# Performance work log

Measured on AMD Instinct MI355X. Metric: run time of the kernel, lower is better.

Reference implementation:

```python
import jax, jax.numpy as jnp
import numpy as np

NHEADS = 16


def setup_inputs() -> dict:
    key = jax.random.key(0)
    ks = jax.random.split(key, 5)
    B, S, D = 2, 2048, 1024
    x = jax.random.normal(ks[0], (B, S, D), dtype=jnp.float32)
    W_packed = jax.random.normal(ks[1], (3 * D, D), dtype=jnp.float32) * (1.0 / np.sqrt(D))
    b_packed = jax.random.normal(ks[2], (3 * D,), dtype=jnp.float32) * 0.02
    W_out = jax.random.normal(ks[3], (D, D), dtype=jnp.float32) * (1.0 / np.sqrt(D))
    b_out = jax.random.normal(ks[4], (D,), dtype=jnp.float32) * 0.02
    return {"x": x, "W_packed": W_packed, "b_packed": b_packed, "W_out": W_out, "b_out": b_out}


def reference(x, W_packed, b_packed, W_out, b_out):
    B, S, D = x.shape
    H = NHEADS
    hd = D // H
    # packed QKV projection (self-attention: q is k is v)
    qkv = x @ W_packed.T + b_packed                       # [B,S,3D]
    q, k, v = jnp.split(qkv, 3, axis=-1)

    def heads(t):
        return t.reshape(B, S, H, hd).transpose(0, 2, 1, 3)  # [B,H,S,hd]

    q, k, v = map(heads, (q, k, v))

    # ALiBi slopes per flex path: exp2(-(h+1)*8/H)
    slopes = jnp.exp2(-(jnp.arange(1, H + 1, dtype=x.dtype) * (8.0 / H)))  # [H]
    pos = jnp.arange(S)
    rel = (pos[None, :] - pos[:, None]).astype(x.dtype)    # kv_idx - q_idx, [S,S]
    bias = slopes[:, None, None] * rel                     # [H,S,S]
    causal = pos[None, :] <= pos[:, None]                  # allowed positions
    neg = jnp.finfo(x.dtype).min
    attn_mask = jnp.where(causal[None, :, :], bias, neg)   # [H,S,S]

    scale = 1.0 / np.sqrt(hd)
    scores = jnp.einsum("bhqd,bhkd->bhqk", q, k) * scale + attn_mask[None]
    attn = jax.nn.softmax(scores, axis=-1)
    out = jnp.einsum("bhqk,bhkd->bhqd", attn, v)           # [B,H,S,hd]
    out = out.transpose(0, 2, 1, 3).reshape(B, S, D)
    return out @ W_out.T + b_out
```

## Files before the change

### kernel.cpp

```cpp
#include <hip/hip_runtime.h>

typedef float f32x4 __attribute__((ext_vector_type(4)));
typedef __bf16 bf16x8 __attribute__((ext_vector_type(8)));
typedef unsigned short u16;

__device__ __forceinline__ f32x4 mfma16(bf16x8 a, bf16x8 b, f32x4 c) {
  return __builtin_amdgcn_mfma_f32_16x16x32_bf16(a, b, c, 0, 0, 0);
}

__device__ __forceinline__ void gll16(const void* g, void* l) {
  __builtin_amdgcn_global_load_lds(
      (const __attribute__((address_space(1))) void*)g,
      (__attribute__((address_space(3))) void*)l, 16, 0, 0);
}

__global__ void cvt3_kernel(const float* __restrict__ x,
                            const float* __restrict__ wp,
                            const float* __restrict__ wo,
                            __bf16* __restrict__ out) {
  int idx = blockIdx.x * blockDim.x + threadIdx.x;
  int stride = gridDim.x * blockDim.x;
  for (int i = idx; i < 1048576; i += stride) {
    const float* src;
    if (i < 524288) src = x + (size_t)i * 8;
    else if (i < 917504) src = wp + (size_t)(i - 524288) * 8;
    else src = wo + (size_t)(i - 917504) * 8;
    f32x4 a = *(const f32x4*)src;
    f32x4 b = *(const f32x4*)(src + 4);
    bf16x8 r;
#pragma unroll
    for (int j = 0; j < 4; ++j) {
      r[j] = (__bf16)a[j];
      r[4 + j] = (__bf16)b[j];
    }
    *(bf16x8*)(out + (size_t)i * 8) = r;
  }
}

template <int BM, int BN, int MODE>
__global__ __launch_bounds__(256, 3) void gemm_bt(
    const u16* __restrict__ A, const u16* __restrict__ B,
    const float* __restrict__ bias, float* __restrict__ Cout,
    __bf16* __restrict__ qb, __bf16* __restrict__ kp, __bf16* __restrict__ vp,
    int M, int N, int K, int mtiles) {
  constexpr int MREP = BM / 32;
  constexpr int NREP = BN / 32;
  constexpr int LA = BM / 64;
  constexpr int LB = BN / 64;
  static_assert(LA + LB == 4, "vmcnt literals assume 4 loads/wave/step");
  __shared__ u16 lA[3 * BM * 32];
  __shared__ u16 lB[3 * BN * 32];
  const int tid = threadIdx.x;
  const int wid = tid >> 6;
  const int lane = tid & 63;
  const int lr = lane & 15;
  const int lg = lane >> 4;

  const int nwg = gridDim.x;
  const int lid = blockIdx.x;
  const int sw = (lid & 7) * (nwg >> 3) + (lid >> 3);
  const int bm = (sw % mtiles) * BM;
  const int bn = (sw / mtiles) * BN;
  const int wm = (wid >> 1) * (BM / 2);
  const int wn = (wid & 1) * (BN / 2);

  f32x4 acc[MREP][NREP] = {};

  auto stage = [&](int bf, int t) {
    const int kt = t * 32;
    char* baseA = (char*)lA + bf * (BM * 64);
    char* baseB = (char*)lB + bf * (BN * 64);
#pragma unroll
    for (int j = 0; j < LA; ++j) {
      int i16 = tid + j * 256;
      int row = i16 >> 2;
      int c = ((i16 & 3) - (row >> 1)) & 3;
      gll16(A + (size_t)(bm + row) * K + kt + c * 8, baseA + i16 * 16);
    }
#pragma unroll
    for (int j = 0; j < LB; ++j) {
      int i16 = tid + j * 256;
      int row = i16 >> 2;
      int c = ((i16 & 3) - (row >> 1)) & 3;
      gll16(B + (size_t)(bn + row) * K + kt + c * 8, baseB + i16 * 16);
    }
  };

  const int T = K / 32;
  stage(0, 0);
  stage(1, 1);
  stage(2, 2);

  const int slotA = ((lg + (lr >> 1)) & 3) * 8;

  for (int t = 0; t < T; ++t) {
    const int rem = T - 1 - t;
    if (rem >= 2)
      asm volatile("s_waitcnt vmcnt(8)" ::: "memory");
    else if (rem == 1)
      asm volatile("s_waitcnt vmcnt(4)" ::: "memory");
    else
      asm volatile("s_waitcnt vmcnt(0)" ::: "memory");
    __builtin_amdgcn_s_barrier();

    const u16* cA = lA + (t % 3) * BM * 32;
    const u16* cB = lB + (t % 3) * BN * 32;
    bf16x8 af[MREP], bfr[NREP];
#pragma unroll
    for (int mt = 0; mt < MREP; ++mt)
      af[mt] = *(const bf16x8*)&cA[(wm + mt * 16 + lr) * 32 + slotA];
#pragma unroll
    for (int nt = 0; nt < NREP; ++nt)
      bfr[nt] = *(const bf16x8*)&cB[(wn + nt * 16 + lr) * 32 + slotA];
#pragma unroll
    for (int mt = 0; mt < MREP; ++mt)
#pragma unroll
      for (int nt = 0; nt < NREP; ++nt)
        acc[mt][nt] = mfma16(af[mt], bfr[nt], acc[mt][nt]);

    __builtin_amdgcn_sched_barrier(0);
    __builtin_amdgcn_s_barrier();
    if (t + 3 < T) stage(t % 3, t + 3);
  }

#pragma unroll
  for (int nt = 0; nt < NREP; ++nt) {
    int col = bn + wn + nt * 16 + lr;
    float bv = bias[col];
#pragma unroll
    for (int mt = 0; mt < MREP; ++mt) {
#pragma unroll
      for (int r = 0; r < 4; ++r) {
        int row = bm + wm + mt * 16 + lg * 4 + r;
        float val = acc[mt][nt][r] + bv;
        if (MODE == 0) {
          Cout[(size_t)row * N + col] = val;
        } else {
          __bf16 bx = (__bf16)val;
          int b = row >> 11, s = row & 2047;
          int third = col >> 10, hd = col & 1023;
          int h = hd >> 6, d = hd & 63;
          if (third == 0) {
            qb[(size_t)row * 1024 + hd] = bx;
          } else {
            int bh = b * 16 + h, t2 = s >> 6, sr = s & 63;
            size_t tb = ((size_t)(bh * 32 + t2)) * 4096;
            if (third == 1)
              kp[tb + (sr >> 4) * 1024 + (d >> 5) * 512 + ((d >> 3) & 3) * 128 +
                 (sr & 15) * 8 + (d & 7)] = bx;
            else
              vp[tb + (d >> 4) * 1024 + (sr >> 5) * 512 + ((sr >> 3) & 3) * 128 +
                 (d & 15) * 8 + (sr & 7)] = bx;
          }
        }
      }
    }
  }
}

__global__ __launch_bounds__(64, 4) void attn_kernel(
    const __bf16* __restrict__ qb, const __bf16* __restrict__ kp,
    const __bf16* __restrict__ vp, __bf16* __restrict__ aout) {
  __shared__ __bf16 p_lds[16][72];
  const int lane = threadIdx.x & 63;
  const int lr = lane & 15;
  const int lg = lane >> 4;

  const int lid = blockIdx.x;
  const int xcd = lid & 7;
  const int rest = lid >> 3;
  const int bh = xcd * 4 + (rest & 3);
  const int a16 = 127 - (rest >> 2);
  const int b = bh >> 4, h = bh & 15;
  const int qr0 = a16 * 16;
  const int ntl = (a16 >> 2) + 1;

  const float LOG2E = 1.4426950408889634f;
  const float c1 = 0.125f * LOG2E;
  const float c2 = exp2f(-(float)(h + 1) * 0.5f) * LOG2E;

  bf16x8 ones;
#pragma unroll
  for (int j = 0; j < 8; ++j) ones[j] = (__bf16)1.0f;

  const u16* ktiles = (const u16*)kp + (size_t)bh * 32 * 4096;
  const u16* vtiles = (const u16*)vp + (size_t)bh * 32 * 4096;

  const __bf16* qrow = qb + (size_t)(b * 2048 + qr0 + lr) * 1024 + h * 64;
  bf16x8 qf0 = *(const bf16x8*)(qrow + lg * 8);
  bf16x8 qf1 = *(const bf16x8*)(qrow + 32 + lg * 8);

  float m[4], l[4], cq[4];
  f32x4 o[4];
#pragma unroll
  for (int r = 0; r < 4; ++r) {
    m[r] = 0.f;
    l[r] = 0.f;
    cq[r] = c2 * (float)(qr0 + lg * 4 + r);
  }
#pragma unroll
  for (int dt = 0; dt < 4; ++dt) o[dt] = (f32x4){0.f, 0.f, 0.f, 0.f};

  for (int t = 0; t < ntl; ++t) {
    const u16* kb = ktiles + (size_t)t * 4096;
    const u16* vb = vtiles + (size_t)t * 4096;
    const int kv = t * 64;
    const bool last = (t == ntl - 1);

    bf16x8 ka[8], va[8];
#pragma unroll
    for (int j = 0; j < 8; ++j)
      ka[j] = *(const bf16x8*)(kb + j * 512 + lane * 8);
#pragma unroll
    for (int j = 0; j < 8; ++j)
      va[j] = *(const bf16x8*)(vb + j * 512 + lane * 8);

    f32x4 s[4];
#pragma unroll
    for (int nt = 0; nt < 4; ++nt) {
      f32x4 tt = (f32x4){0.f, 0.f, 0.f, 0.f};
      tt = mfma16(qf0, ka[nt * 2], tt);
      tt = mfma16(qf1, ka[nt * 2 + 1], tt);
      s[nt] = tt;
    }

#pragma unroll
    for (int nt = 0; nt < 4; ++nt) {
      float bnt = c2 * (float)(kv + nt * 16 + lr);
#pragma unroll
      for (int r = 0; r < 4; ++r)
        s[nt][r] = __builtin_fmaf(s[nt][r], c1, bnt - cq[r]);
    }
    if (last) {
#pragma unroll
      for (int nt = 0; nt < 4; ++nt) {
        float kf = (float)(kv + nt * 16 + lr);
#pragma unroll
        for (int r = 0; r < 4; ++r) {
          float qi = (float)(qr0 + lg * 4 + r);
          if (kf > qi) s[nt][r] = -1e30f;
        }
      }
    }

    float pm[4];
#pragma unroll
    for (int r = 0; r < 4; ++r)
      pm[r] = fmaxf(fmaxf(s[0][r], s[1][r]), fmaxf(s[2][r], s[3][r]));
    bool ok = (pm[0] <= m[0] + 8.f) && (pm[1] <= m[1] + 8.f) &&
              (pm[2] <= m[2] + 8.f) && (pm[3] <= m[3] + 8.f);
    if (!__all(ok)) {
#pragma unroll
      for (int r = 0; r < 4; ++r)
#pragma unroll
        for (int d = 1; d < 16; d <<= 1)
          pm[r] = fmaxf(pm[r], __shfl_xor(pm[r], d));
#pragma unroll
      for (int r = 0; r < 4; ++r) {
        float mn = fmaxf(m[r], pm[r]);
        float fac = __builtin_amdgcn_exp2f(m[r] - mn);
        m[r] = mn;
        l[r] *= fac;
#pragma unroll
        for (int dt = 0; dt < 4; ++dt) o[dt][r] *= fac;
      }
    }

#pragma unroll
    for (int nt = 0; nt < 4; ++nt)
#pragma unroll
      for (int r = 0; r < 4; ++r) {
        float e = __builtin_amdgcn_exp2f(s[nt][r] - m[r]);
        p_lds[lg * 4 + r][nt * 16 + lr] = (__bf16)e;
      }

    bf16x8 pa0 = *(const bf16x8*)&p_lds[lr][lg * 8];
    bf16x8 pa1 = *(const bf16x8*)&p_lds[lr][32 + lg * 8];

    {
      f32x4 tt = (f32x4){0.f, 0.f, 0.f, 0.f};
      tt = mfma16(pa0, ones, tt);
      tt = mfma16(pa1, ones, tt);
#pragma unroll
      for (int r = 0; r < 4; ++r) l[r] += tt[r];
    }

#pragma unroll
    for (int dt = 0; dt < 4; ++dt) {
      o[dt] = mfma16(pa0, va[dt * 2], o[dt]);
      o[dt] = mfma16(pa1, va[dt * 2 + 1], o[dt]);
    }
  }

#pragma unroll
  for (int dt = 0; dt < 4; ++dt)
#pragma unroll
    for (int r = 0; r < 4; ++r) {
      float val = o[dt][r] / l[r];
      aout[(size_t)(b * 2048 + qr0 + lg * 4 + r) * 1024 + h * 64 + dt * 16 + lr] =
          (__bf16)val;
    }
}

extern "C" void kernel_launch(void* const* d_in, const int* in_sizes, int n_in,
                              void* d_out, int out_size, void* d_ws, size_t ws_size,
                              hipStream_t stream) {
  (void)in_sizes; (void)n_in; (void)out_size; (void)ws_size;
  const float* x = (const float*)d_in[0];
  const float* Wp = (const float*)d_in[1];
  const float* bp = (const float*)d_in[2];
  const float* Wo = (const float*)d_in[3];
  const float* bo = (const float*)d_in[4];
  float* out = (float*)d_out;

  char* ws = (char*)d_ws;
  u16* xb  = (u16*)(ws);
  u16* wpb = (u16*)(ws + (size_t)(8u << 20));
  u16* wob = (u16*)(ws + (size_t)(14u << 20));
  u16* qbp = (u16*)(ws + (size_t)(16u << 20));
  u16* kpp = (u16*)(ws + (size_t)(24u << 20));
  u16* vpp = (u16*)(ws + (size_t)(32u << 20));
  u16* ab  = xb;

  cvt3_kernel<<<2048, 256, 0, stream>>>(x, Wp, Wo, (__bf16*)xb);
  gemm_bt<128, 128, 1><<<768, 256, 0, stream>>>(
      xb, wpb, bp, nullptr, (__bf16*)qbp, (__bf16*)kpp, (__bf16*)vpp,
      4096, 3072, 1024, 32);
  attn_kernel<<<4096, 64, 0, stream>>>(
      (const __bf16*)qbp, (const __bf16*)kpp, (const __bf16*)vpp, (__bf16*)ab);
  gemm_bt<128, 128, 0><<<256, 256, 0, stream>>>(
      ab, wob, bo, out, nullptr, nullptr, nullptr, 4096, 1024, 1024, 32);
}
```

Before: 115.0 us.

## Process two 16-row query groups per attention wave to reuse K/V tiles

Each attention wavefront now handles 32 query rows (two 16-row groups) instead of 16, so every K/V tile loaded from global memory feeds twice as many MFMAs. The grid is halved to 2048 blocks and launch bounds drop to 2 waves per SIMD, trading occupancy for more registers. MFMA sections are also wrapped in s_setprio to raise wave priority during matrix work. The risks are lower latency hiding and coarser causal load balance, since the last tile now holds more masked work.

```diff
diff --git a/kernel.cpp b/kernel.cpp
--- a/kernel.cpp
+++ b/kernel.cpp
@@ -158,10 +158,10 @@
   }
 }
 
-__global__ __launch_bounds__(64, 4) void attn_kernel(
+__global__ __launch_bounds__(64, 2) void attn_kernel(
     const __bf16* __restrict__ qb, const __bf16* __restrict__ kp,
     const __bf16* __restrict__ vp, __bf16* __restrict__ aout) {
-  __shared__ __bf16 p_lds[16][72];
+  __shared__ __bf16 p_lds[2][16][72];
   const int lane = threadIdx.x & 63;
   const int lr = lane & 15;
   const int lg = lane >> 4;
@@ -170,10 +170,10 @@
   const int xcd = lid & 7;
   const int rest = lid >> 3;
   const int bh = xcd * 4 + (rest & 3);
-  const int a16 = 127 - (rest >> 2);
+  const int a32 = 63 - (rest >> 2);
   const int b = bh >> 4, h = bh & 15;
-  const int qr0 = a16 * 16;
-  const int ntl = (a16 >> 2) + 1;
+  const int qr0 = a32 * 32;
+  const int ntl = (a32 >> 1) + 1;
 
   const float LOG2E = 1.4426950408889634f;
   const float c1 = 0.125f * LOG2E;
@@ -186,20 +186,26 @@
   const u16* ktiles = (const u16*)kp + (size_t)bh * 32 * 4096;
   const u16* vtiles = (const u16*)vp + (size_t)bh * 32 * 4096;
 
-  const __bf16* qrow = qb + (size_t)(b * 2048 + qr0 + lr) * 1024 + h * 64;
-  bf16x8 qf0 = *(const bf16x8*)(qrow + lg * 8);
-  bf16x8 qf1 = *(const bf16x8*)(qrow + 32 + lg * 8);
-
-  float m[4], l[4], cq[4];
-  f32x4 o[4];
-#pragma unroll
-  for (int r = 0; r < 4; ++r) {
-    m[r] = 0.f;
-    l[r] = 0.f;
-    cq[r] = c2 * (float)(qr0 + lg * 4 + r);
-  }
-#pragma unroll
-  for (int dt = 0; dt < 4; ++dt) o[dt] = (f32x4){0.f, 0.f, 0.f, 0.f};
+  bf16x8 qf[2][2];
+#pragma unroll
+  for (int g = 0; g < 2; ++g) {
+    const __bf16* qrow =
+        qb + (size_t)(b * 2048 + qr0 + g * 16 + lr) * 1024 + h * 64;
+    qf[g][0] = *(const bf16x8*)(qrow + lg * 8);
+    qf[g][1] = *(const bf16x8*)(qrow + 32 + lg * 8);
+  }
+
+  float m[2][4], l[2][4], cq[2][4];
+  f32x4 o[2][4];
+#pragma unroll
+  for (int g = 0; g < 2; ++g)
+#pragma unroll
+    for (int r = 0; r < 4; ++r) {
+      m[g][r] = 0.f;
+      l[g][r] = 0.f;
+      cq[g][r] = c2 * (float)(qr0 + g * 16 + lg * 4 + r);
+      o[g][r] = (f32x4){0.f, 0.f, 0.f, 0.f};
+    }
 
   for (int t = 0; t < ntl; ++t) {
     const u16* kb = ktiles + (size_t)t * 4096;
@@ -215,91 +221,121 @@
     for (int j = 0; j < 8; ++j)
       va[j] = *(const bf16x8*)(vb + j * 512 + lane * 8);
 
-    f32x4 s[4];
-#pragma unroll
-    for (int nt = 0; nt < 4; ++nt) {
-      f32x4 tt = (f32x4){0.f, 0.f, 0.f, 0.f};
-      tt = mfma16(qf0, ka[nt * 2], tt);
-      tt = mfma16(qf1, ka[nt * 2 + 1], tt);
-      s[nt] = tt;
-    }
+    f32x4 s[2][4];
+    __builtin_amdgcn_s_setprio(1);
+#pragma unroll
+    for (int g = 0; g < 2; ++g)
+#pragma unroll
+      for (int nt = 0; nt < 4; ++nt) {
+        f32x4 tt = (f32x4){0.f, 0.f, 0.f, 0.f};
+        tt = mfma16(qf[g][0], ka[nt * 2], tt);
+        tt = mfma16(qf[g][1], ka[nt * 2 + 1], tt);
+        s[g][nt] = tt;
+      }
+    __builtin_amdgcn_s_setprio(0);
 
 #pragma unroll
     for (int nt = 0; nt < 4; ++nt) {
       float bnt = c2 * (float)(kv + nt * 16 + lr);
 #pragma unroll
-      for (int r = 0; r < 4; ++r)
-        s[nt][r] = __builtin_fmaf(s[nt][r], c1, bnt - cq[r]);
+      for (int g = 0; g < 2; ++g)
+#pragma unroll
+        for (int r = 0; r < 4; ++r)
+          s[g][nt][r] = __builtin_fmaf(s[g][nt][r], c1, bnt - cq[g][r]);
     }
     if (last) {
 #pragma unroll
       for (int nt = 0; nt < 4; ++nt) {
         float kf = (float)(kv + nt * 16 + lr);
 #pragma unroll
+        for (int g = 0; g < 2; ++g)
+#pragma unroll
+          for (int r = 0; r < 4; ++r) {
+            float qi = (float)(qr0 + g * 16 + lg * 4 + r);
+            if (kf > qi) s[g][nt][r] = -1e30f;
+          }
+      }
+    }
+
+    float pm[2][4];
+#pragma unroll
+    for (int g = 0; g < 2; ++g)
+#pragma unroll
+      for (int r = 0; r < 4; ++r)
+        pm[g][r] =
+            fmaxf(fmaxf(s[g][0][r], s[g][1][r]), fmaxf(s[g][2][r], s[g][3][r]));
+    bool ok = true;
+#pragma unroll
+    for (int g = 0; g < 2; ++g)
+#pragma unroll
+      for (int r = 0; r < 4; ++r) ok = ok && (pm[g][r] <= m[g][r] + 8.f);
+    if (!__all(ok)) {
+#pragma unroll
+      for (int g = 0; g < 2; ++g)
+#pragma unroll
+        for (int r = 0; r < 4; ++r)
+#pragma unroll
+          for (int d = 1; d < 16; d <<= 1)
+            pm[g][r] = fmaxf(pm[g][r], __shfl_xor(pm[g][r], d));
+#pragma unroll
+      for (int g = 0; g < 2; ++g)
+#pragma unroll
         for (int r = 0; r < 4; ++r) {
-          float qi = (float)(qr0 + lg * 4 + r);
-          if (kf > qi) s[nt][r] = -1e30f;
+          float mn = fmaxf(m[g][r], pm[g][r]);
+          float fac = __builtin_amdgcn_exp2f(m[g][r] - mn);
+          m[g][r] = mn;
+          l[g][r] *= fac;
+#pragma unroll
+          for (int dt = 0; dt < 4; ++dt) o[g][dt][r] *= fac;
         }
-      }
-    }
-
-    float pm[4];
-#pragma unroll
-    for (int r = 0; r < 4; ++r)
-      pm[r] = fmaxf(fmaxf(s[0][r], s[1][r]), fmaxf(s[2][r], s[3][r]));
-    bool ok = (pm[0] <= m[0] + 8.f) && (pm[1] <= m[1] + 8.f) &&
-              (pm[2] <= m[2] + 8.f) && (pm[3] <= m[3] + 8.f);
-    if (!__all(ok)) {
-#pragma unroll
-      for (int r = 0; r < 4; ++r)
-#pragma unroll
-        for (int d = 1; d < 16; d <<= 1)
-          pm[r] = fmaxf(pm[r], __shfl_xor(pm[r], d));
+    }
+
+#pragma unroll
+    for (int g = 0; g < 2; ++g)
+#pragma unroll
+      for (int nt = 0; nt < 4; ++nt)
+#pragma unroll
+        for (int r = 0; r < 4; ++r) {
+          float e = __builtin_amdgcn_exp2f(s[g][nt][r] - m[g][r]);
+          p_lds[g][lg * 4 + r][nt * 16 + lr] = (__bf16)e;
+        }
+
+    bf16x8 pa[2][2];
+#pragma unroll
+    for (int g = 0; g < 2; ++g) {
+      pa[g][0] = *(const bf16x8*)&p_lds[g][lr][lg * 8];
+      pa[g][1] = *(const bf16x8*)&p_lds[g][lr][32 + lg * 8];
+    }
+
+    __builtin_amdgcn_s_setprio(1);
+#pragma unroll
+    for (int g = 0; g < 2; ++g) {
+      f32x4 tt = (f32x4){0.f, 0.f, 0.f, 0.f};
+      tt = mfma16(pa[g][0], ones, tt);
+      tt = mfma16(pa[g][1], ones, tt);
+#pragma unroll
+      for (int r = 0; r < 4; ++r) l[g][r] += tt[r];
+    }
+#pragma unroll
+    for (int g = 0; g < 2; ++g)
+#pragma unroll
+      for (int dt = 0; dt < 4; ++dt) {
+        o[g][dt] = mfma16(pa[g][0], va[dt * 2], o[g][dt]);
+        o[g][dt] = mfma16(pa[g][1], va[dt * 2 + 1], o[g][dt]);
+      }
+    __builtin_amdgcn_s_setprio(0);
+  }
+
+#pragma unroll
+  for (int g = 0; g < 2; ++g)
+#pragma unroll
+    for (int dt = 0; dt < 4; ++dt)
 #pragma unroll
       for (int r = 0; r < 4; ++r) {
-        float mn = fmaxf(m[r], pm[r]);
-        float fac = __builtin_amdgcn_exp2f(m[r] - mn);
-        m[r] = mn;
-        l[r] *= fac;
-#pragma unroll
-        for (int dt = 0; dt < 4; ++dt) o[dt][r] *= fac;
-      }
-    }
-
-#pragma unroll
-    for (int nt = 0; nt < 4; ++nt)
-#pragma unroll
-      for (int r = 0; r < 4; ++r) {
-        float e = __builtin_amdgcn_exp2f(s[nt][r] - m[r]);
-        p_lds[lg * 4 + r][nt * 16 + lr] = (__bf16)e;
-      }
-
-    bf16x8 pa0 = *(const bf16x8*)&p_lds[lr][lg * 8];
-    bf16x8 pa1 = *(const bf16x8*)&p_lds[lr][32 + lg * 8];
-
-    {
-      f32x4 tt = (f32x4){0.f, 0.f, 0.f, 0.f};
-      tt = mfma16(pa0, ones, tt);
-      tt = mfma16(pa1, ones, tt);
-#pragma unroll
-      for (int r = 0; r < 4; ++r) l[r] += tt[r];
-    }
-
-#pragma unroll
-    for (int dt = 0; dt < 4; ++dt) {
-      o[dt] = mfma16(pa0, va[dt * 2], o[dt]);
-      o[dt] = mfma16(pa1, va[dt * 2 + 1], o[dt]);
-    }
-  }
-
-#pragma unroll
-  for (int dt = 0; dt < 4; ++dt)
-#pragma unroll
-    for (int r = 0; r < 4; ++r) {
-      float val = o[dt][r] / l[r];
-      aout[(size_t)(b * 2048 + qr0 + lg * 4 + r) * 1024 + h * 64 + dt * 16 + lr] =
-          (__bf16)val;
-    }
+        float val = o[g][dt][r] / l[g][r];
+        aout[(size_t)(b * 2048 + qr0 + g * 16 + lg * 4 + r) * 1024 + h * 64 +
+             dt * 16 + lr] = (__bf16)val;
+      }
 }
 
 extern "C" void kernel_launch(void* const* d_in, const int* in_sizes, int n_in,
@@ -326,7 +362,7 @@
   gemm_bt<128, 128, 1><<<768, 256, 0, stream>>>(
       xb, wpb, bp, nullptr, (__bf16*)qbp, (__bf16*)kpp, (__bf16*)vpp,
       4096, 3072, 1024, 32);
-  attn_kernel<<<4096, 64, 0, stream>>>(
+  attn_kernel<<<2048, 64, 0, stream>>>(
       (const __bf16*)qbp, (const __bf16*)kpp, (const __bf16*)vpp, (__bf16*)ab);
   gemm_bt<128, 128, 0><<<256, 256, 0, stream>>>(
       ab, wob, bo, out, nullptr, nullptr, nullptr, 4096, 1024, 1024, 32);
```

New measurement: 118.9 us. 3.4% more time.
